# Kernel optimization log

Hardware: AMD Instinct MI355X
Metric: run time of the kernel (lower is better)

## Reference

```python
import jax, jax.numpy as jnp
import numpy as np

HAD_G = 32  # hadamard_group_size == MX block size (scales are [out, in//32])

# FP4 E2M1 magnitude grid and decision midpoints (round-to-nearest)
_FP4_LEVELS = jnp.array([0.0, 0.5, 1.0, 1.5, 2.0, 3.0, 4.0, 6.0], dtype=jnp.float32)
_FP4_MIDS = jnp.array([0.25, 0.75, 1.25, 1.75, 2.5, 3.5, 5.0], dtype=jnp.float32)


def _hadamard(n: int) -> np.ndarray:
    H = np.array([[1.0]], dtype=np.float32)
    while H.shape[0] < n:
        H = np.block([[H, H], [H, -H]])
    return H * (n ** -0.5)


def mxfp4_quant_dequant(v):
    """MXFP4 quantize-dequantize along the last axis (block of 32).
    v: [..., 32]. Shared power-of-2 scale per block (E8M0, absmax-based),
    elements rounded to nearest FP4 (E2M1) value. Straight-through estimator.
    """
    amax = jnp.max(jnp.abs(v), axis=-1, keepdims=True)
    # scale = 2^(floor(log2(amax)) - emax_fp4), emax_fp4 = 2 (6 = 1.5 * 2^2)
    e = jnp.floor(jnp.log2(jnp.maximum(amax, jnp.float32(1e-30)))) - 2.0
    scale = jnp.exp2(e)
    a = v / scale
    mag = jnp.minimum(jnp.abs(a), 6.0)
    q = _FP4_LEVELS[jnp.digitize(mag, _FP4_MIDS)] * jnp.sign(a)
    deq = q * scale
    # STE: identity gradient through the quantizer (matches custom autograd Fn)
    return v + jax.lax.stop_gradient(deq - v)


def _rotate_quant(t, H):
    """Per-group Hadamard rotation then MXFP4 quant-dequant. t: [N, K]."""
    N, K = t.shape
    tg = t.reshape(N, K // HAD_G, HAD_G)
    tr = jnp.einsum('ngh,hk->ngk', tg, H)  # rotate each 32-group
    return mxfp4_quant_dequant(tr).reshape(N, K)


def setup_inputs() -> dict:
    key = jax.random.key(0)
    kx, kw, kb = jax.random.split(key, 3)
    B, S, K, O = 4, 2048, 4096, 16384
    x = jax.random.normal(kx, (B, S, K), dtype=jnp.float32)
    weight = jax.random.normal(kw, (O, K), dtype=jnp.float32) * 0.02
    bias = jax.random.normal(kb, (O,), dtype=jnp.float32) * 0.01
    fwd_hadamard = jnp.asarray(_hadamard(HAD_G))
    return {"x": x, "weight": weight, "bias": bias, "fwd_hadamard": fwd_hadamard}


def reference(x, weight, bias, fwd_hadamard):
    B, S, K = x.shape
    O = weight.shape[0]
    xq = _rotate_quant(x.reshape(B * S, K), fwd_hadamard)   # deq(q(x H))
    wq = _rotate_quant(weight, fwd_hadamard)                # deq(q(W H))
    # H H^T = I, so (xH)(WH)^T approximates x W^T; GEMM runs on quantized values
    y = xq @ wq.T + bias
    return y.reshape(B, S, O)
```

## Files before the change

### kernel.cpp

```cpp
#include <hip/hip_runtime.h>

typedef unsigned short u16;
typedef unsigned int u32;
typedef unsigned char u8;
typedef int v8i __attribute__((ext_vector_type(8)));
typedef int v4i __attribute__((ext_vector_type(4)));
typedef float v16f __attribute__((ext_vector_type(16)));

#define INV_SQRT32 0.17677669529663688f

#define QOFS_OUT 32768
#define QOFS_SC  36864

__global__ __launch_bounds__(256) void rotquant4_kernel(
    const float* __restrict__ T, u8* __restrict__ Q4, u8* __restrict__ S,
    int K, int ntk, int nkb )
{
    __shared__ __align__(16) u8 smem[37120];

    const int tid  = threadIdx.x;
    const int bid  = blockIdx.x;
    const int rblk = bid / nkb;
    const int kblk = bid - rblk * nkb;
    const int row0 = rblk * 8;
    const int kb0  = kblk * 32;
    const int t0g  = (row0 >> 7) * ntk + (kb0 >> 2);
    const int rl   = row0 & 127;

    {
        const float4* src = (const float4*)T;
#pragma unroll
        for (int j = 0; j < 8; ++j) {
            float4 t = src[(size_t)(row0 + j) * (K >> 2) + (kblk << 8) + tid];
            int kb = tid >> 3, i = tid & 7;
            *(float4*)(smem + j * 4096 + kb * 128 + ((i ^ (kb & 7)) << 4)) = t;
        }
    }
    __syncthreads();

    {
        const int rr = tid >> 5;
        const int kb = tid & 31;

        float v[32];
#pragma unroll
        for (int i = 0; i < 8; ++i) {
            float4 t = *(const float4*)(smem + rr * 4096 + kb * 128
                                        + ((i ^ (kb & 7)) << 4));
            v[i*4+0] = t.x; v[i*4+1] = t.y; v[i*4+2] = t.z; v[i*4+3] = t.w;
        }

#pragma unroll
        for (int s = 1; s < 32; s <<= 1) {
#pragma unroll
            for (int i = 0; i < 32; ++i) {
                if (!(i & s)) {
                    float a = v[i], b = v[i | s];
                    v[i] = a + b;
                    v[i | s] = a - b;
                }
            }
        }

        float amax = 0.f;
#pragma unroll
        for (int i = 0; i < 32; ++i) {
            v[i] *= INV_SQRT32;
            amax = fmaxf(amax, fabsf(v[i]));
        }

        u32 ab = __float_as_uint(amax);
        int be = (int)(ab >> 23);
        u32 w[4] = {0u, 0u, 0u, 0u};
        u8 sbyte = 0;
        if (be >= 3) {
            sbyte = (u8)(be - 2);
            float iscale = __uint_as_float((u32)(256 - be) << 23);
#pragma unroll
            for (int i = 0; i < 32; ++i) {
                float a = v[i] * iscale;
                float m = fminf(fabsf(a), 6.0f);
                int c = (m < 0.25f) ? 0 :
                        (m < 0.75f) ? 1 :
                        (m < 1.25f) ? 2 :
                        (m < 1.75f) ? 3 :
                        (m < 2.5f)  ? 4 :
                        (m < 3.5f)  ? 5 :
                        (m < 5.0f)  ? 6 : 7;
                c |= (int)((__float_as_uint(a) >> 28) & 8u);
                w[i >> 3] |= (u32)c << (4 * (i & 7));
            }
        }

        uint4 p; p.x = w[0]; p.y = w[1]; p.z = w[2]; p.w = w[3];
        *(uint4*)(smem + QOFS_OUT + rr * 512 + (kb >> 2) * 64 + (kb & 3) * 16) = p;
        smem[QOFS_SC + rr * 32 + (kb >> 2) * 4 + (kb & 3)] = sbyte;
    }
    __syncthreads();

    {
        int tileL = tid >> 5, slot = (tid >> 3) & 3, rr = tid & 7;
        uint4 p = *(const uint4*)(smem + QOFS_OUT + rr * 512 + tileL * 64
                                  + slot * 16);
        ((uint4*)Q4)[(size_t)(t0g + tileL) * 512 + slot * 128 + rl + rr] = p;
    }
    if (tid < 64) {
        int tileL = tid >> 3, rr = tid & 7;
        u32 sc = *(const u32*)(smem + QOFS_SC + rr * 32 + tileL * 4);
        ((u32*)S)[(size_t)(t0g + tileL) * 128 + rl + rr] = sc;
    }
}

__device__ __forceinline__ void gload16(const void* g, void* l)
{
    __builtin_amdgcn_global_load_lds(
        (__attribute__((address_space(1))) void*)g,
        (__attribute__((address_space(3))) void*)l, 16, 0, 0);
}
__device__ __forceinline__ void gload4(const void* g, void* l)
{
    __builtin_amdgcn_global_load_lds(
        (__attribute__((address_space(1))) void*)g,
        (__attribute__((address_space(3))) void*)l, 4, 0, 0);
}

#define BUF_BYTES 34816
#define OFS_B     16384
#define OFS_AS    32768
#define OFS_BS    33792
#define BB0 0
#define BB1 BUF_BYTES
#define BB2 (2 * BUF_BYTES)

__global__ __launch_bounds__(512, 2) void gemm4_bias(
    const u8* __restrict__ A4, const u8* __restrict__ AS,
    const u8* __restrict__ B4, const u8* __restrict__ BS,
    const float* __restrict__ bias, float* __restrict__ C,
    int M, int N, int K)
{
    __shared__ __align__(16) u8 smem[3 * BUF_BYTES];

    const int tid  = threadIdx.x;
    const int wave = tid >> 6;
    const int lane = tid & 63;
    const int l31  = lane & 31;
    const int lhi  = lane >> 5;
    const int wm   = wave >> 2;
    const int wn   = wave & 3;
    const int ntk  = K >> 7;
    const int NT   = ntk;

    const int nbn = N >> 8;
    const int nbm = M >> 8;
    int bid = blockIdx.x;
    int bm, bn;
    if (((gridDim.x & 7) == 0) && ((nbm & 7) == 0)) {
        int bpc = nbm >> 3;
        int lb  = __builtin_ctz(bpc);
        int c   = bid & 7;
        int r   = bid >> 3;
        bm = c * bpc + (r & (bpc - 1));
        bn = r >> lb;
    } else {
        bn = bid % nbn;
        bm = bid / nbn;
    }

    v16f acc[4][2];
#pragma unroll
    for (int i = 0; i < 4; ++i)
#pragma unroll
        for (int j = 0; j < 2; ++j)
#pragma unroll
            for (int r = 0; r < 16; ++r) acc[i][j][r] = 0.f;

    const size_t aRow0 = (size_t)(2 * bm) * ntk;
    const size_t bRow0 = (size_t)(2 * bn) * ntk;
    const int isA = (wave < 4);
    const int w4  = wave & 3;
    const u8* scB = isA ? AS : BS;
    const size_t scT = (size_t)((isA ? 2 * bm : 2 * bn) + (w4 >> 1)) * ntk;
    const int scInner = (w4 & 1) * 256 + lane * 4;
    const int scDst   = (isA ? OFS_AS : OFS_BS) + w4 * 256;
    const int gOfs = wave * 1024 + lane * 16;
    const int lOfs = wave * 1024;

    const int aRB   = wm * 8192 + lhi * 2048 + l31 * 16;
    const int bRB   = OFS_B + (wn >> 1) * 8192 + lhi * 2048
                      + (wn & 1) * 1024 + l31 * 16;
    const int asB   = OFS_AS + wm * 512 + l31 * 4;
    const int bsB   = OFS_BS + wn * 256 + l31 * 4;
    const int shamt = lhi * 8;

#define STG_A(bofs, kt, r)                                                    \
    gload16(A4 + ((aRow0 + (size_t)(r) * ntk + (kt)) << 13) + gOfs,           \
            smem + (bofs) + (r) * 8192 + lOfs)
#define STG_B(bofs, kt, r)                                                    \
    gload16(B4 + ((bRow0 + (size_t)(r) * ntk + (kt)) << 13) + gOfs,           \
            smem + (bofs) + OFS_B + (r) * 8192 + lOfs)
#define STG_S(bofs, kt)                                                       \
    gload4(scB + ((scT + (kt)) << 9) + scInner, smem + (bofs) + scDst)
#define STAGE(bofs, kt)                                                       \
    do { STG_A(bofs, kt, 0); STG_A(bofs, kt, 1);                              \
         STG_B(bofs, kt, 0); STG_B(bofs, kt, 1); STG_S(bofs, kt); } while (0)

#define MK8(x) __builtin_shufflevector(x, x, 0, 1, 2, 3, -1, -1, -1, -1)
#define MFMA1(mi, ni, AF, BF, SA, SB)                                         \
    acc[mi][ni] = __builtin_amdgcn_mfma_scale_f32_32x32x64_f8f6f4(            \
        MK8(AF), MK8(BF), acc[mi][ni], 4, 4, 0, (int)(SA), 0, (int)(SB))
#define CL8(A0, A1, A2, A3, Bx0, Bx1, S0, S1, S2, S3, T0, T1)                 \
    do {                                                                      \
        MFMA1(0, 0, A0, Bx0, S0, T0); MFMA1(0, 1, A0, Bx1, S0, T1);           \
        MFMA1(1, 0, A1, Bx0, S1, T0); MFMA1(1, 1, A1, Bx1, S1, T1);           \
        MFMA1(2, 0, A2, Bx0, S2, T0); MFMA1(2, 1, A2, Bx1, S2, T1);           \
        MFMA1(3, 0, A3, Bx0, S3, T0); MFMA1(3, 1, A3, Bx1, S3, T1);           \
    } while (0)

#define TILE(CO, PO, kt, ST, FINAL)                                           \
    do {                                                                      \
        if (ST) STAGE(PO, (kt) + 2);                                          \
        u32 sa0 = (*(const u32*)(smem + (CO) + asB      )) >> shamt;          \
        u32 sa1 = (*(const u32*)(smem + (CO) + asB + 128)) >> shamt;          \
        u32 sa2 = (*(const u32*)(smem + (CO) + asB + 256)) >> shamt;          \
        u32 sa3 = (*(const u32*)(smem + (CO) + asB + 384)) >> shamt;          \
        u32 sb0 = (*(const u32*)(smem + (CO) + bsB      )) >> shamt;          \
        u32 sb1 = (*(const u32*)(smem + (CO) + bsB + 128)) >> shamt;          \
        v4i a00 = *(const v4i*)(smem + (CO) + aRB       );                    \
        v4i a01 = *(const v4i*)(smem + (CO) + aRB +  512);                    \
        v4i a02 = *(const v4i*)(smem + (CO) + aRB + 1024);                    \
        v4i a03 = *(const v4i*)(smem + (CO) + aRB + 1536);                    \
        v4i b00 = *(const v4i*)(smem + (CO) + bRB       );                    \
        v4i b01 = *(const v4i*)(smem + (CO) + bRB +  512);                    \
        v4i a10 = *(const v4i*)(smem + (CO) + aRB + 4096);                    \
        v4i a11 = *(const v4i*)(smem + (CO) + aRB + 4608);                    \
        v4i a12 = *(const v4i*)(smem + (CO) + aRB + 5120);                    \
        v4i a13 = *(const v4i*)(smem + (CO) + aRB + 5632);                    \
        v4i b10 = *(const v4i*)(smem + (CO) + bRB + 4096);                    \
        v4i b11 = *(const v4i*)(smem + (CO) + bRB + 4608);                    \
        __builtin_amdgcn_s_setprio(1);                                        \
        CL8(a00, a01, a02, a03, b00, b01,                                     \
            sa0 & 0xffu, sa1 & 0xffu, sa2 & 0xffu, sa3 & 0xffu,               \
            sb0 & 0xffu, sb1 & 0xffu);                                        \
        CL8(a10, a11, a12, a13, b10, b11,                                     \
            (sa0 >> 16) & 0xffu, (sa1 >> 16) & 0xffu,                         \
            (sa2 >> 16) & 0xffu, (sa3 >> 16) & 0xffu,                         \
            (sb0 >> 16) & 0xffu, (sb1 >> 16) & 0xffu);                        \
        __builtin_amdgcn_s_setprio(0);                                        \
        if (!(FINAL)) {                                                       \
            if (ST) { asm volatile("s_waitcnt vmcnt(5)" ::: "memory"); }      \
            else    { asm volatile("s_waitcnt vmcnt(0)" ::: "memory"); }      \
            __builtin_amdgcn_s_barrier();                                     \
        }                                                                     \
    } while (0)

    STAGE(BB0, 0);
    STAGE(BB1, 1);
    asm volatile("s_waitcnt vmcnt(5)" ::: "memory");
    __builtin_amdgcn_s_barrier();

#pragma unroll 1
    for (int t = 0; t + 2 < NT; t += 3) {
        TILE(BB0, BB2, t + 0, true, false);
        TILE(BB1, BB0, t + 1, true, false);
        TILE(BB2, BB1, t + 2, true, false);
    }
    TILE(BB0, BB2, NT - 2, false, false);
    TILE(BB1, BB2, NT - 1, false, true);

    const int cb = bn * 256 + wn * 64;
    const int rb = bm * 256 + wm * 128;
#pragma unroll
    for (int ni = 0; ni < 2; ++ni) {
        float bb = bias[cb + ni * 32 + l31];
#pragma unroll
        for (int mi = 0; mi < 4; ++mi) {
#pragma unroll
            for (int reg = 0; reg < 16; ++reg) {
                int row = (reg & 3) + 8 * (reg >> 2) + 4 * lhi;
                C[(size_t)(rb + mi * 32 + row) * N + cb + ni * 32 + l31]
                    = acc[mi][ni][reg] + bb;
            }
        }
    }
#undef STG_A
#undef STG_B
#undef STG_S
#undef STAGE
#undef MK8
#undef MFMA1
#undef CL8
#undef TILE
}

extern "C" void kernel_launch(void* const* d_in, const int* in_sizes, int n_in,
                              void* d_out, int out_size, void* d_ws, size_t ws_size,
                              hipStream_t stream)
{
    const float* x    = (const float*)d_in[0];
    const float* w    = (const float*)d_in[1];
    const float* bias = (const float*)d_in[2];

    const int O = in_sizes[2];
    const int K = in_sizes[1] / O;
    const int M = in_sizes[0] / K;

    u8* x4 = (u8*)d_ws;
    u8* w4 = x4 + (size_t)M * (K / 2);
    u8* xs = w4 + (size_t)O * (K / 2);
    u8* ws = xs + (size_t)M * (K / 32);

    const int ntk = K / 128;
    const int nkb = K / 1024;
    rotquant4_kernel<<<(M / 8) * nkb, 256, 0, stream>>>(x, x4, xs, K, ntk, nkb);
    rotquant4_kernel<<<(O / 8) * nkb, 256, 0, stream>>>(w, w4, ws, K, ntk, nkb);

    dim3 grid((M / 256) * (O / 256));
    gemm4_bias<<<grid, 512, 0, stream>>>(x4, xs, w4, ws, bias, (float*)d_out,
                                         M, O, K);
}
```

Measured before the change: 454.7 us.

## Software-pipeline LDS fragment loads across barrier and relayout scale bytes

Reorganizes the GEMM main loop so LDS fragment loads interleave with MFMAs. The second half-K MFMAs now run after the barrier, while the next tile's scales and first A/B fragments are prefetched into registers. The quantizer kernel writes scale words in a permuted order, so each lane can fetch all its scales with one 16-byte (A) or 8-byte (B) LDS read instead of several 4-byte reads. The intent is to hide LDS latency behind matrix-core work and cut the number of LDS instructions, at the cost of extra live registers and a tighter coupling of the scale layout between the two kernels.

```diff
diff --git a/kernel.cpp b/kernel.cpp
--- a/kernel.cpp
+++ b/kernel.cpp
@@ -5,6 +5,7 @@
 typedef unsigned char u8;
 typedef int v8i __attribute__((ext_vector_type(8)));
 typedef int v4i __attribute__((ext_vector_type(4)));
+typedef int v2i __attribute__((ext_vector_type(2)));
 typedef float v16f __attribute__((ext_vector_type(16)));
 
 #define INV_SQRT32 0.17677669529663688f
@@ -107,7 +108,9 @@
     if (tid < 64) {
         int tileL = tid >> 3, rr = tid & 7;
         u32 sc = *(const u32*)(smem + QOFS_SC + rr * 32 + tileL * 4);
-        ((u32*)S)[(size_t)(t0g + tileL) * 128 + rl + rr] = sc;
+        int r7 = rl + rr;
+        ((u32*)S)[(size_t)(t0g + tileL) * 128 + ((r7 & 31) << 2)
+                  + ((r7 >> 5) & 3)] = sc;
     }
 }
 
@@ -185,12 +188,13 @@
     const int gOfs = wave * 1024 + lane * 16;
     const int lOfs = wave * 1024;
 
-    const int aRB   = wm * 8192 + lhi * 2048 + l31 * 16;
-    const int bRB   = OFS_B + (wn >> 1) * 8192 + lhi * 2048
-                      + (wn & 1) * 1024 + l31 * 16;
-    const int asB   = OFS_AS + wm * 512 + l31 * 4;
-    const int bsB   = OFS_BS + wn * 256 + l31 * 4;
-    const int shamt = lhi * 8;
+    const int aRB = wm * 8192 + lhi * 2048 + l31 * 16;
+    const int bRB = OFS_B + (wn >> 1) * 8192 + lhi * 2048
+                    + (wn & 1) * 1024 + l31 * 16;
+    const int asB = OFS_AS + wm * 512 + l31 * 16;
+    const int bsB = OFS_BS + (wn >> 1) * 512 + (wn & 1) * 8 + l31 * 16;
+    const int sh0 = lhi * 8;
+    const int sh1 = sh0 + 16;
 
 #define STG_A(bofs, kt, r)                                                    \
     gload16(A4 + ((aRow0 + (size_t)(r) * ntk + (kt)) << 13) + gOfs,           \
@@ -208,49 +212,54 @@
 #define MFMA1(mi, ni, AF, BF, SA, SB)                                         \
     acc[mi][ni] = __builtin_amdgcn_mfma_scale_f32_32x32x64_f8f6f4(            \
         MK8(AF), MK8(BF), acc[mi][ni], 4, 4, 0, (int)(SA), 0, (int)(SB))
-#define CL8(A0, A1, A2, A3, Bx0, Bx1, S0, S1, S2, S3, T0, T1)                 \
-    do {                                                                      \
-        MFMA1(0, 0, A0, Bx0, S0, T0); MFMA1(0, 1, A0, Bx1, S0, T1);           \
-        MFMA1(1, 0, A1, Bx0, S1, T0); MFMA1(1, 1, A1, Bx1, S1, T1);           \
-        MFMA1(2, 0, A2, Bx0, S2, T0); MFMA1(2, 1, A2, Bx1, S2, T1);           \
-        MFMA1(3, 0, A3, Bx0, S3, T0); MFMA1(3, 1, A3, Bx1, S3, T1);           \
-    } while (0)
-
-#define TILE(CO, PO, kt, ST, FINAL)                                           \
+
+#define TILE(CO, NO, PO, kt, ST, REFILL, FINAL)                               \
     do {                                                                      \
         if (ST) STAGE(PO, (kt) + 2);                                          \
-        u32 sa0 = (*(const u32*)(smem + (CO) + asB      )) >> shamt;          \
-        u32 sa1 = (*(const u32*)(smem + (CO) + asB + 128)) >> shamt;          \
-        u32 sa2 = (*(const u32*)(smem + (CO) + asB + 256)) >> shamt;          \
-        u32 sa3 = (*(const u32*)(smem + (CO) + asB + 384)) >> shamt;          \
-        u32 sb0 = (*(const u32*)(smem + (CO) + bsB      )) >> shamt;          \
-        u32 sb1 = (*(const u32*)(smem + (CO) + bsB + 128)) >> shamt;          \
-        v4i a00 = *(const v4i*)(smem + (CO) + aRB       );                    \
-        v4i a01 = *(const v4i*)(smem + (CO) + aRB +  512);                    \
-        v4i a02 = *(const v4i*)(smem + (CO) + aRB + 1024);                    \
-        v4i a03 = *(const v4i*)(smem + (CO) + aRB + 1536);                    \
-        v4i b00 = *(const v4i*)(smem + (CO) + bRB       );                    \
-        v4i b01 = *(const v4i*)(smem + (CO) + bRB +  512);                    \
+                       \
+        u32 ya0 = ((u32)SAv[0] >> sh0) & 0xffu;                               \
+        u32 ya1 = ((u32)SAv[1] >> sh0) & 0xffu;                               \
+        u32 ya2 = ((u32)SAv[2] >> sh0) & 0xffu;                               \
+        u32 ya3 = ((u32)SAv[3] >> sh0) & 0xffu;                               \
+        u32 yb0 = ((u32)SBv[0] >> sh0) & 0xffu;                               \
+        u32 yb1 = ((u32)SBv[1] >> sh0) & 0xffu;                               \
+        u32 xa0 = ((u32)SAv[0] >> sh1) & 0xffu;                               \
+        u32 xa1 = ((u32)SAv[1] >> sh1) & 0xffu;                               \
+        u32 xa2 = ((u32)SAv[2] >> sh1) & 0xffu;                               \
+        u32 xa3 = ((u32)SAv[3] >> sh1) & 0xffu;                               \
+        u32 xb0 = ((u32)SBv[0] >> sh1) & 0xffu;                               \
+        u32 xb1 = ((u32)SBv[1] >> sh1) & 0xffu;                               \
+        __builtin_amdgcn_s_setprio(1);                                        \
+        v4i a2 = *(const v4i*)(smem + (CO) + aRB + 1024);                     \
+        v4i a3 = *(const v4i*)(smem + (CO) + aRB + 1536);                     \
+        MFMA1(0, 0, A0a, B0a, ya0, yb0); MFMA1(0, 1, A0a, B0b, ya0, yb1);     \
+        v4i b1a = *(const v4i*)(smem + (CO) + bRB + 4096);                    \
+        v4i b1b = *(const v4i*)(smem + (CO) + bRB + 4608);                    \
+        MFMA1(1, 0, A0b, B0a, ya1, yb0); MFMA1(1, 1, A0b, B0b, ya1, yb1);     \
         v4i a10 = *(const v4i*)(smem + (CO) + aRB + 4096);                    \
         v4i a11 = *(const v4i*)(smem + (CO) + aRB + 4608);                    \
+        MFMA1(2, 0, a2, B0a, ya2, yb0); MFMA1(2, 1, a2, B0b, ya2, yb1);       \
         v4i a12 = *(const v4i*)(smem + (CO) + aRB + 5120);                    \
         v4i a13 = *(const v4i*)(smem + (CO) + aRB + 5632);                    \
-        v4i b10 = *(const v4i*)(smem + (CO) + bRB + 4096);                    \
-        v4i b11 = *(const v4i*)(smem + (CO) + bRB + 4608);                    \
-        __builtin_amdgcn_s_setprio(1);                                        \
-        CL8(a00, a01, a02, a03, b00, b01,                                     \
-            sa0 & 0xffu, sa1 & 0xffu, sa2 & 0xffu, sa3 & 0xffu,               \
-            sb0 & 0xffu, sb1 & 0xffu);                                        \
-        CL8(a10, a11, a12, a13, b10, b11,                                     \
-            (sa0 >> 16) & 0xffu, (sa1 >> 16) & 0xffu,                         \
-            (sa2 >> 16) & 0xffu, (sa3 >> 16) & 0xffu,                         \
-            (sb0 >> 16) & 0xffu, (sb1 >> 16) & 0xffu);                        \
+        MFMA1(3, 0, a3, B0a, ya3, yb0); MFMA1(3, 1, a3, B0b, ya3, yb1);       \
         __builtin_amdgcn_s_setprio(0);                                        \
         if (!(FINAL)) {                                                       \
             if (ST) { asm volatile("s_waitcnt vmcnt(5)" ::: "memory"); }      \
             else    { asm volatile("s_waitcnt vmcnt(0)" ::: "memory"); }      \
             __builtin_amdgcn_s_barrier();                                     \
         }                                                                     \
+        __builtin_amdgcn_s_setprio(1);                                        \
+        if (REFILL) { SAv = *(const v4i*)(smem + (NO) + asB);                 \
+                      SBv = *(const v2i*)(smem + (NO) + bsB); }               \
+        MFMA1(0, 0, a10, b1a, xa0, xb0); MFMA1(0, 1, a10, b1b, xa0, xb1);     \
+        if (REFILL) { B0a = *(const v4i*)(smem + (NO) + bRB);                 \
+                      B0b = *(const v4i*)(smem + (NO) + bRB + 512); }         \
+        MFMA1(1, 0, a11, b1a, xa1, xb0); MFMA1(1, 1, a11, b1b, xa1, xb1);     \
+        if (REFILL) { A0a = *(const v4i*)(smem + (NO) + aRB);                 \
+                      A0b = *(const v4i*)(smem + (NO) + aRB + 512); }         \
+        MFMA1(2, 0, a12, b1a, xa2, xb0); MFMA1(2, 1, a12, b1b, xa2, xb1);     \
+        MFMA1(3, 0, a13, b1a, xa3, xb0); MFMA1(3, 1, a13, b1b, xa3, xb1);     \
+        __builtin_amdgcn_s_setprio(0);                                        \
     } while (0)
 
     STAGE(BB0, 0);
@@ -258,14 +267,21 @@
     asm volatile("s_waitcnt vmcnt(5)" ::: "memory");
     __builtin_amdgcn_s_barrier();
 
+    v4i SAv = *(const v4i*)(smem + BB0 + asB);
+    v2i SBv = *(const v2i*)(smem + BB0 + bsB);
+    v4i B0a = *(const v4i*)(smem + BB0 + bRB);
+    v4i B0b = *(const v4i*)(smem + BB0 + bRB + 512);
+    v4i A0a = *(const v4i*)(smem + BB0 + aRB);
+    v4i A0b = *(const v4i*)(smem + BB0 + aRB + 512);
+
 #pragma unroll 1
     for (int t = 0; t + 2 < NT; t += 3) {
-        TILE(BB0, BB2, t + 0, true, false);
-        TILE(BB1, BB0, t + 1, true, false);
-        TILE(BB2, BB1, t + 2, true, false);
-    }
-    TILE(BB0, BB2, NT - 2, false, false);
-    TILE(BB1, BB2, NT - 1, false, true);
+        TILE(BB0, BB1, BB2, t + 0, true, true, false);
+        TILE(BB1, BB2, BB0, t + 1, true, true, false);
+        TILE(BB2, BB0, BB1, t + 2, true, true, false);
+    }
+    TILE(BB0, BB1, BB2, NT - 2, false, true, false);
+    TILE(BB1, BB2, BB0, NT - 1, false, false, true);
 
     const int cb = bn * 256 + wn * 64;
     const int rb = bm * 256 + wm * 128;
@@ -288,7 +304,6 @@
 #undef STAGE
 #undef MK8
 #undef MFMA1
-#undef CL8
 #undef TILE
 }
 
```

New measurement: 441.3 us. 1.03x faster.
